# Kernel tuning notes

Hardware: AMD Instinct MI355X
Metric: run time of the kernel (lower is better)

The kernel has to match this reference:

```python
import jax, jax.numpy as jnp
import numpy as np
import math

B, S, D, H = 4, 2048, 512, 8
HD = D // H

def setup_inputs() -> dict:
    key = jax.random.key(0)
    ks = jax.random.split(key, 12)
    s_hd = 1.0 / math.sqrt(HD)
    s_d = 1.0 / math.sqrt(D)
    return {
        "q": jax.random.normal(ks[0], (B, S, D), jnp.float32),
        "k": jax.random.normal(ks[1], (B, S, D), jnp.float32),
        "v": jax.random.normal(ks[2], (B, S, D), jnp.float32),
        # torch nn.Linear(head_dim, head_dim): weight [HD, HD], bias [HD]
        "Wq": jax.random.uniform(ks[3], (HD, HD), jnp.float32, -s_hd, s_hd),
        "bq": jax.random.uniform(ks[4], (HD,), jnp.float32, -s_hd, s_hd),
        "Wk": jax.random.uniform(ks[5], (HD, HD), jnp.float32, -s_hd, s_hd),
        "bk": jax.random.uniform(ks[6], (HD,), jnp.float32, -s_hd, s_hd),
        "Wv": jax.random.uniform(ks[7], (HD, HD), jnp.float32, -s_hd, s_hd),
        "bv": jax.random.uniform(ks[8], (HD,), jnp.float32, -s_hd, s_hd),
        # output projection nn.Linear(d, d)
        "Wo": jax.random.uniform(ks[9], (D, D), jnp.float32, -s_d, s_d),
        "bo": jax.random.uniform(ks[10], (D,), jnp.float32, -s_d, s_d),
        # LayerNorm(d) affine params
        "gamma": jnp.ones((D,), jnp.float32),
        "beta": jnp.zeros((D,), jnp.float32),
    }

def _layernorm(x, gamma, beta, eps=1e-5):
    mu = jnp.mean(x, axis=-1, keepdims=True)
    var = jnp.var(x, axis=-1, keepdims=True)
    return (x - mu) * jax.lax.rsqrt(var + eps) * gamma + beta

def reference(q, k, v, Wq, bq, Wk, bk, Wv, bv, Wo, bo, gamma, beta):
    batch, q_len = q.shape[0], q.shape[1]
    # split heads: [B, L, H, HD]; per-head Linear shares one weight across heads
    Qh = q.reshape(batch, q_len, H, HD) @ Wq.T + bq
    Kh = k.reshape(batch, k.shape[1], H, HD) @ Wk.T + bk
    Vh = v.reshape(batch, v.shape[1], H, HD) @ Wv.T + bv
    # scores scaled by sqrt(d) (faithful to source, NOT sqrt(head_dim))
    scores = jnp.einsum('bqhd,bkhd->bhqk', Qh, Kh) / math.sqrt(D)
    attn = jax.nn.softmax(scores, axis=-1)
    out = jnp.einsum('bhqk,bkhd->bqhd', attn, Vh)
    concat = out.reshape(batch, q_len, D)
    lin = concat @ Wo.T + bo
    # AddNorm quirk: residual added AFTER LayerNorm (dropout = identity in eval)
    return q + _layernorm(lin, gamma, beta)
```

## Files before the change

kernel.cpp:

```cpp
#include <hip/hip_runtime.h>
#include <hip/hip_bf16.h>
#include <math.h>
#include <stdint.h>

#define B 4
#define S 2048
#define D 512
#define H 8
#define HD 64

typedef __attribute__((ext_vector_type(4))) int   int4v;
typedef __attribute__((ext_vector_type(8))) short short8;
typedef __attribute__((ext_vector_type(4))) short short4v;
typedef __attribute__((ext_vector_type(4))) float f32x4;

__device__ __forceinline__ unsigned short bfr(float x) {
    __bf16 h = (__bf16)x;
    union { __bf16 b; unsigned short s; } u; u.b = h; return u.s;
}
__device__ __forceinline__ float b2f(unsigned short s) {
    union { unsigned u; float f; } v; v.u = (unsigned)s << 16; return v.f;
}
__device__ __forceinline__ float ex2(float x) {
#if __has_builtin(__builtin_amdgcn_exp2f)
    return __builtin_amdgcn_exp2f(x);
#else
    return exp2f(x);
#endif
}
__device__ __forceinline__ short8 cvt8(const float* p) {
    float4 f0 = *(const float4*)p;
    float4 f1 = *(const float4*)(p + 4);
    short8 s8;
    s8[0] = (short)bfr(f0.x); s8[1] = (short)bfr(f0.y);
    s8[2] = (short)bfr(f0.z); s8[3] = (short)bfr(f0.w);
    s8[4] = (short)bfr(f1.x); s8[5] = (short)bfr(f1.y);
    s8[6] = (short)bfr(f1.z); s8[7] = (short)bfr(f1.w);
    return s8;
}

#define QSCALE 0.06377229601488305f
#define MFIX 4.0f

typedef const __attribute__((address_space(1))) unsigned char g8_t;
typedef __attribute__((address_space(3))) unsigned char l8_t;
__device__ __forceinline__ void gl_lds16(const unsigned short* g, unsigned short* l) {
#if __has_builtin(__builtin_amdgcn_global_load_lds)
    __builtin_amdgcn_global_load_lds((g8_t*)g, (l8_t*)l, 16, 0, 0);
#else
    int lane = threadIdx.x & 63;
    ((int4v*)l)[lane] = *(const int4v*)g;
#endif
}

__global__ __launch_bounds__(256) void qkv_mfma_kernel(
    const float* __restrict__ q, const float* __restrict__ k,
    const float* __restrict__ v,
    const float* __restrict__ Wq, const float* __restrict__ bq,
    const float* __restrict__ Wk, const float* __restrict__ bk,
    const float* __restrict__ Wv, const float* __restrict__ bv,
    const float* __restrict__ Wo, unsigned short* __restrict__ WoB,
    unsigned short* __restrict__ Qh, unsigned short* __restrict__ Kh,
    unsigned short* __restrict__ VtG)
{
    const int t = threadIdx.x;
    if (blockIdx.x >= 3072) {
        int i = (blockIdx.x - 3072) * 1024 + t * 4;
        float4 f = *(const float4*)(Wo + i);
        short4v s;
        s[0] = (short)bfr(f.x); s[1] = (short)bfr(f.y);
        s[2] = (short)bfr(f.z); s[3] = (short)bfr(f.w);
        *(short4v*)(WoB + i) = s;
        return;
    }

    const int L = t & 63, w = t >> 6;
    const int c = L & 15, qd = L >> 4;
    const int task = blockIdx.x * 4 + w;
    const int st = task & 127;
    const int h  = (task >> 7) & 7;
    const int b  = (task >> 10) & 3;
    const int x  = task >> 12;

    const float* Wf     = (x == 0) ? Wq : (x == 1) ? Wk : Wv;
    const float* bias_p = (x == 0) ? bq : (x == 1) ? bk : bv;
    const float* X      = (x == 0) ? q  : (x == 1) ? k  : v;

    const float* xrow = X + ((size_t)(b * S + st * 16 + c)) * D + h * HD;
    short8 af[2];
    #pragma unroll
    for (int kc = 0; kc < 2; ++kc) af[kc] = cvt8(xrow + kc * 32 + 8 * qd);

    if (x < 2) {
        f32x4 acc[4];
        #pragma unroll
        for (int nt = 0; nt < 4; ++nt) {
            float bv_ = bias_p[16 * nt + c];
            acc[nt] = (f32x4){bv_, bv_, bv_, bv_};
            short8 b0 = cvt8(Wf + (16 * nt + c) * HD + 8 * qd);
            short8 b1 = cvt8(Wf + (16 * nt + c) * HD + 32 + 8 * qd);
            acc[nt] = __builtin_amdgcn_mfma_f32_16x16x32_bf16(af[0], b0, acc[nt], 0, 0, 0);
            acc[nt] = __builtin_amdgcn_mfma_f32_16x16x32_bf16(af[1], b1, acc[nt], 0, 0, 0);
        }
        unsigned short* O = ((x == 0) ? Qh : Kh)
                          + ((size_t)(b * H + h) * S + st * 16) * HD;
        const float sc = (x == 0) ? QSCALE : 1.0f;
        #pragma unroll
        for (int nt = 0; nt < 4; ++nt)
            #pragma unroll
            for (int r = 0; r < 4; ++r)
                O[(4 * qd + r) * HD + 16 * nt + c] = bfr(acc[nt][r] * sc);
    } else {
        f32x4 acc[4];
        #pragma unroll
        for (int nt = 0; nt < 4; ++nt) {
            float4 bb4 = *(const float4*)(bias_p + 16 * nt + 4 * qd);
            acc[nt] = (f32x4){bb4.x, bb4.y, bb4.z, bb4.w};
            short8 a0 = cvt8(Wf + (16 * nt + c) * HD + 8 * qd);
            short8 a1 = cvt8(Wf + (16 * nt + c) * HD + 32 + 8 * qd);
            acc[nt] = __builtin_amdgcn_mfma_f32_16x16x32_bf16(a0, af[0], acc[nt], 0, 0, 0);
            acc[nt] = __builtin_amdgcn_mfma_f32_16x16x32_bf16(a1, af[1], acc[nt], 0, 0, 0);
        }
        unsigned short* O = VtG + (size_t)(b * H + h) * HD * S;
        #pragma unroll
        for (int nt = 0; nt < 4; ++nt)
            #pragma unroll
            for (int r = 0; r < 4; ++r)
                O[(size_t)(16 * nt + 4 * qd + r) * S + st * 16 + c] = bfr(acc[nt][r]);
    }
}

__global__ __launch_bounds__(256, 4) void attn_kernel(
    const unsigned short* __restrict__ Qh, const unsigned short* __restrict__ Kh,
    const unsigned short* __restrict__ VtG, unsigned short* __restrict__ accPb,
    float* __restrict__ lP)
{
    __shared__ __align__(16) unsigned short Ks[2][4096];
    __shared__ __align__(16) unsigned short Vs[2][4096];

    const int idx = blockIdx.x;
    const int bh = idx & 31;
    const int rem = idx >> 5;
    const int qt = rem >> 1;
    const int ks = rem & 1;
    const int b = bh >> 3, h = bh & 7;
    const int t = threadIdx.x;
    const int w = t >> 6, L = t & 63;
    const int c = L & 15, qd = L >> 4;

    const unsigned short* Kb = Kh + ((size_t)bh * S + ks * 1024) * HD;
    const unsigned short* Vb = VtG + (size_t)bh * HD * S + ks * 1024;

    short8 qf[2][2];
    #pragma unroll
    for (int qg = 0; qg < 2; ++qg)
        #pragma unroll
        for (int kc = 0; kc < 2; ++kc)
            qf[qg][kc] = *(const short8*)(Qh
                + ((size_t)bh * S + qt * 128 + w * 32 + qg * 16 + c) * HD
                + kc * 32 + 8 * qd);

    f32x4 acc[2][4];
    float lrun[2] = {0.f, 0.f};
    #pragma unroll
    for (int qg = 0; qg < 2; ++qg)
        #pragma unroll
        for (int dt = 0; dt < 4; ++dt) acc[qg][dt] = (f32x4){0.f, 0.f, 0.f, 0.f};

    const int sd = t >> 3, sj = t & 7;
    const int sp = sj >> 2, smt = (sj >> 1) & 1;
    const int sqa = (2 * sj) & 3, sqb = (2 * sj + 1) & 3;

    int4v vpre[2];
    #pragma unroll
    for (int i = 0; i < 2; ++i) {
        int bi = w + 4 * i;
        gl_lds16(Kb + (size_t)(16 * (bi >> 1) + c) * HD + (bi & 1) * 32 + qd * 8,
                 &Ks[0][bi * 512]);
        vpre[i] = *(const int4v*)(Vb + (size_t)(sd + 32 * i) * S + 8 * sj);
    }

    for (int it = 0; it < 16; ++it) {
        const int cur = it & 1, nxt = cur ^ 1;
        #pragma unroll
        for (int i = 0; i < 2; ++i) {
            int d = sd + 32 * i;
            int dt = d >> 4, cc = d & 15;
            union { int4v v; short4v h[2]; } u; u.v = vpre[i];
            *(short4v*)&Vs[cur][((dt * 2 + sp) * 64 + sqa * 16 + cc) * 8 + smt * 4] = u.h[0];
            *(short4v*)&Vs[cur][((dt * 2 + sp) * 64 + sqb * 16 + cc) * 8 + smt * 4] = u.h[1];
        }
        __syncthreads();
        if (it + 1 < 16) {
            int n1 = (it + 1) * 64;
            #pragma unroll
            for (int i = 0; i < 2; ++i) {
                int bi = w + 4 * i;
                gl_lds16(Kb + (size_t)(n1 + 16 * (bi >> 1) + c) * HD + (bi & 1) * 32 + qd * 8,
                         &Ks[nxt][bi * 512]);
                vpre[i] = *(const int4v*)(Vb + (size_t)(sd + 32 * i) * S + n1 + 8 * sj);
            }
        }

        const unsigned short* KsC = Ks[cur];
        const unsigned short* VsC = Vs[cur];

        short4v pa[2][4];
        #pragma unroll
        for (int mt = 0; mt < 4; ++mt) {
            short8 a0 = *(const short8*)(KsC + (mt * 2 + 0) * 512 + L * 8);
            short8 a1 = *(const short8*)(KsC + (mt * 2 + 1) * 512 + L * 8);
            #pragma unroll
            for (int qg = 0; qg < 2; ++qg) {
                f32x4 stv = (f32x4){-MFIX, -MFIX, -MFIX, -MFIX};
                stv = __builtin_amdgcn_mfma_f32_16x16x32_bf16(a0, qf[qg][0], stv, 0, 0, 0);
                stv = __builtin_amdgcn_mfma_f32_16x16x32_bf16(a1, qf[qg][1], stv, 0, 0, 0);
                float p0 = ex2(stv[0]), p1 = ex2(stv[1]);
                float p2 = ex2(stv[2]), p3 = ex2(stv[3]);
                lrun[qg] += (p0 + p1) + (p2 + p3);
                short4v p_;
                p_[0] = (short)bfr(p0); p_[1] = (short)bfr(p1);
                p_[2] = (short)bfr(p2); p_[3] = (short)bfr(p3);
                pa[qg][mt] = p_;
            }
        }

        #pragma unroll
        for (int dt = 0; dt < 4; ++dt)
            #pragma unroll
            for (int p = 0; p < 2; ++p) {
                union { short8 v8; short4v h[2]; } u;
                u.v8 = *(const short8*)(VsC + (dt * 2 + p) * 512 + L * 8);
#if __has_builtin(__builtin_amdgcn_mfma_f32_16x16x16bf16_1k)
                #pragma unroll
                for (int qg = 0; qg < 2; ++qg) {
                    acc[qg][dt] = __builtin_amdgcn_mfma_f32_16x16x16bf16_1k(
                        pa[qg][2 * p + 0], u.h[0], acc[qg][dt], 0, 0, 0);
                    acc[qg][dt] = __builtin_amdgcn_mfma_f32_16x16x16bf16_1k(
                        pa[qg][2 * p + 1], u.h[1], acc[qg][dt], 0, 0, 0);
                }
#else
                #pragma unroll
                for (int qg = 0; qg < 2; ++qg) {
                    short8 pz0 = {pa[qg][2 * p + 0][0], pa[qg][2 * p + 0][1],
                                  pa[qg][2 * p + 0][2], pa[qg][2 * p + 0][3], 0, 0, 0, 0};
                    short8 pz1 = {pa[qg][2 * p + 1][0], pa[qg][2 * p + 1][1],
                                  pa[qg][2 * p + 1][2], pa[qg][2 * p + 1][3], 0, 0, 0, 0};
                    short8 v0 = {u.h[0][0], u.h[0][1], u.h[0][2], u.h[0][3], 0, 0, 0, 0};
                    short8 v1 = {u.h[1][0], u.h[1][1], u.h[1][2], u.h[1][3], 0, 0, 0, 0};
                    acc[qg][dt] = __builtin_amdgcn_mfma_f32_16x16x32_bf16(pz0, v0, acc[qg][dt], 0, 0, 0);
                    acc[qg][dt] = __builtin_amdgcn_mfma_f32_16x16x32_bf16(pz1, v1, acc[qg][dt], 0, 0, 0);
                }
#endif
            }
    }

    const int q0 = qt * 128 + w * 32;
    unsigned short* accPp = accPb + (size_t)ks * ((size_t)B * S * D)
                          + ((size_t)b * S + q0) * D + h * HD;
    #pragma unroll
    for (int qg = 0; qg < 2; ++qg) {
        float lr = lrun[qg];
        lr += __shfl_xor(lr, 16);
        lr += __shfl_xor(lr, 32);
        if (qd == 0)
            lP[(size_t)ks * ((size_t)B * H * S) + (size_t)bh * S + q0 + qg * 16 + c] = lr;
        #pragma unroll
        for (int dt = 0; dt < 4; ++dt)
            #pragma unroll
            for (int r = 0; r < 4; ++r)
                accPp[(size_t)(qg * 16 + 4 * qd + r) * D + 16 * dt + c]
                    = bfr(acc[qg][dt][r]);
    }
}

__global__ __launch_bounds__(512) void oproj_ln_kernel(
    const unsigned short* __restrict__ accPb, const float* __restrict__ lP,
    const unsigned short* __restrict__ WoB,
    const float* __restrict__ bo, const float* __restrict__ gamma,
    const float* __restrict__ beta, const float* __restrict__ qin,
    float* __restrict__ out)
{
    __shared__ __align__(16) unsigned short As[16 * 520];
    __shared__ float red[2][8][16];
    __shared__ float linv_s[16][8];

    const int t = threadIdx.x;
    const int r0 = blockIdx.x * 16;
    const int w = t >> 6, L = t & 63;
    const int c = L & 15, qd = L >> 4;
    const int n0 = w * 64;
    const size_t NEh = (size_t)B * S * D;
    const size_t BHS = (size_t)B * H * S;

    if (t < 128) {
        int row = t >> 3, hh = t & 7;
        int bb = r0 >> 11;
        int ss = (r0 & (S - 1)) + row;
        float l0 = lP[(size_t)(bb * H + hh) * S + ss];
        float l1 = lP[BHS + (size_t)(bb * H + hh) * S + ss];
        linv_s[row][hh] = 1.f / (l0 + l1);
    }
    __syncthreads();

    #pragma unroll
    for (int i = 0; i < 4; ++i) {
        int flat = t + 512 * i;
        int row = flat >> 7, cg = flat & 127;
        int col = cg * 4;
        size_t gi = (size_t)(r0 + row) * D + col;
        short4v a0 = *(const short4v*)(accPb + gi);
        short4v a1 = *(const short4v*)(accPb + NEh + gi);
        float li = linv_s[row][col >> 6];
        short4v s;
        #pragma unroll
        for (int j = 0; j < 4; ++j)
            s[j] = (short)bfr((b2f((unsigned short)a0[j])
                             + b2f((unsigned short)a1[j])) * li);
        *(short4v*)&As[row * 520 + col] = s;
    }
    __syncthreads();

    f32x4 acc[4];
    #pragma unroll
    for (int nt = 0; nt < 4; ++nt) {
        float bv_ = bo[n0 + 16 * nt + c];
        acc[nt] = (f32x4){bv_, bv_, bv_, bv_};
    }

    for (int kc = 0; kc < 16; ++kc) {
        short8 a0 = *(const short8*)&As[c * 520 + kc * 32 + 8 * qd];
        #pragma unroll
        for (int nt = 0; nt < 4; ++nt) {
            short8 bf = *(const short8*)(WoB + (size_t)(n0 + 16 * nt + c) * D
                                         + kc * 32 + 8 * qd);
            acc[nt] = __builtin_amdgcn_mfma_f32_16x16x32_bf16(a0, bf, acc[nt], 0, 0, 0);
        }
    }

    float sm[4], sq[4];
    #pragma unroll
    for (int r = 0; r < 4; ++r) { sm[r] = 0.f; sq[r] = 0.f; }
    #pragma unroll
    for (int nt = 0; nt < 4; ++nt)
        #pragma unroll
        for (int r = 0; r < 4; ++r) {
            float x_ = acc[nt][r];
            sm[r] += x_; sq[r] += x_ * x_;
        }
    #pragma unroll
    for (int mask = 1; mask <= 8; mask <<= 1)
        #pragma unroll
        for (int r = 0; r < 4; ++r) {
            sm[r] += __shfl_xor(sm[r], mask);
            sq[r] += __shfl_xor(sq[r], mask);
        }
    if (c == 0) {
        #pragma unroll
        for (int r = 0; r < 4; ++r) {
            red[0][w][4 * qd + r] = sm[r];
            red[1][w][4 * qd + r] = sq[r];
        }
    }
    __syncthreads();

    float mu[4], rs[4];
    #pragma unroll
    for (int r = 0; r < 4; ++r) {
        int m_ = 4 * qd + r;
        float s_ = 0.f, q_ = 0.f;
        #pragma unroll
        for (int w_ = 0; w_ < 8; ++w_) { s_ += red[0][w_][m_]; q_ += red[1][w_][m_]; }
        float mu_ = s_ * (1.f / D);
        float var = q_ * (1.f / D) - mu_ * mu_;
        mu[r] = mu_;
        rs[r] = rsqrtf(var + 1e-5f);
    }

    #pragma unroll
    for (int nt = 0; nt < 4; ++nt) {
        int n = n0 + 16 * nt + c;
        float g = gamma[n], be = beta[n];
        #pragma unroll
        for (int r = 0; r < 4; ++r) {
            size_t gi = (size_t)(r0 + 4 * qd + r) * D + n;
            out[gi] = qin[gi] + (acc[nt][r] - mu[r]) * rs[r] * g + be;
        }
    }
}

extern "C" void kernel_launch(void* const* d_in, const int* in_sizes, int n_in,
                              void* d_out, int out_size, void* d_ws, size_t ws_size,
                              hipStream_t stream) {
    const float* q     = (const float*)d_in[0];
    const float* k     = (const float*)d_in[1];
    const float* v     = (const float*)d_in[2];
    const float* Wq    = (const float*)d_in[3];
    const float* bq    = (const float*)d_in[4];
    const float* Wk    = (const float*)d_in[5];
    const float* bk    = (const float*)d_in[6];
    const float* Wv    = (const float*)d_in[7];
    const float* bv    = (const float*)d_in[8];
    const float* Wo    = (const float*)d_in[9];
    const float* bo    = (const float*)d_in[10];
    const float* gamma = (const float*)d_in[11];
    const float* beta  = (const float*)d_in[12];
    float* out = (float*)d_out;

    const size_t NE = (size_t)B * S * D;
    unsigned short* wsu = (unsigned short*)d_ws;
    unsigned short* Qh    = wsu;
    unsigned short* Kh    = wsu + NE;
    unsigned short* VtG   = wsu + 2 * NE;
    unsigned short* WoB   = wsu + 3 * NE;
    unsigned short* accPb = WoB + (size_t)D * D;
    float* lP = (float*)(accPb + 2 * NE);

    hipLaunchKernelGGL(qkv_mfma_kernel, dim3(3072 + 256), dim3(256), 0, stream,
                       q, k, v, Wq, bq, Wk, bk, Wv, bv, Wo, WoB, Qh, Kh, VtG);
    hipLaunchKernelGGL(attn_kernel, dim3(1024), dim3(256), 0, stream,
                       Qh, Kh, VtG, accPb, lP);
    hipLaunchKernelGGL(oproj_ln_kernel, dim3(B * S / 16), dim3(512), 0, stream,
                       accPb, lP, WoB, bo, gamma, beta, q, out);
}
```

Measured before the change: 217.6 us.

## Stage QKV weights in LDS and double row tile in output projection

In the QKV kernel, each block now loads and converts the 64x64 weight into shared memory once and keeps the bf16 fragments in registers. Each wave then processes two 16-row tiles, so the grid halves and the repeated per-wave global weight loads go away. The output-projection/LayerNorm kernel now handles 32 rows per block with 1024 threads, so each Wo fragment feeds two MFMAs, and the row-stat reduction moves to shared memory with an extra barrier. The trade-offs are a larger block size and fewer blocks, which may lower occupancy and load balance.

Result: faster. 192.5 us (-11.6%).

```diff
diff --git a/kernel.cpp b/kernel.cpp
--- a/kernel.cpp
+++ b/kernel.cpp
@@ -64,8 +64,9 @@
     unsigned short* __restrict__ VtG)
 {
     const int t = threadIdx.x;
-    if (blockIdx.x >= 3072) {
-        int i = (blockIdx.x - 3072) * 1024 + t * 4;
+    const int bid = blockIdx.x;
+    if (bid >= 1536) {
+        int i = (bid - 1536) * 1024 + t * 4;
         float4 f = *(const float4*)(Wo + i);
         short4v s;
         s[0] = (short)bfr(f.x); s[1] = (short)bfr(f.y);
@@ -74,59 +75,90 @@
         return;
     }
 
+    __shared__ __align__(16) unsigned short Wl[64 * 72];
+
+    const int x   = bid / 512;
+    const int r_  = bid - x * 512;
+    const int bh  = r_ >> 4;
+    const int stg = r_ & 15;
+    const int b = bh >> 3, h = bh & 7;
     const int L = t & 63, w = t >> 6;
     const int c = L & 15, qd = L >> 4;
-    const int task = blockIdx.x * 4 + w;
-    const int st = task & 127;
-    const int h  = (task >> 7) & 7;
-    const int b  = (task >> 10) & 3;
-    const int x  = task >> 12;
 
     const float* Wf     = (x == 0) ? Wq : (x == 1) ? Wk : Wv;
     const float* bias_p = (x == 0) ? bq : (x == 1) ? bk : bv;
     const float* X      = (x == 0) ? q  : (x == 1) ? k  : v;
 
-    const float* xrow = X + ((size_t)(b * S + st * 16 + c)) * D + h * HD;
-    short8 af[2];
-    #pragma unroll
-    for (int kc = 0; kc < 2; ++kc) af[kc] = cvt8(xrow + kc * 32 + 8 * qd);
+    {
+        int base = t * 16;
+        int row = t >> 2, col = (t & 3) * 16;
+        short8 s0 = cvt8(Wf + base);
+        short8 s1 = cvt8(Wf + base + 8);
+        *(short8*)&Wl[row * 72 + col]     = s0;
+        *(short8*)&Wl[row * 72 + col + 8] = s1;
+    }
+    __syncthreads();
+
+    short8 wf[4][2];
+    #pragma unroll
+    for (int nt = 0; nt < 4; ++nt)
+        #pragma unroll
+        for (int kc = 0; kc < 2; ++kc)
+            wf[nt][kc] = *(const short8*)&Wl[(16 * nt + c) * 72 + kc * 32 + 8 * qd];
 
     if (x < 2) {
-        f32x4 acc[4];
-        #pragma unroll
-        for (int nt = 0; nt < 4; ++nt) {
-            float bv_ = bias_p[16 * nt + c];
-            acc[nt] = (f32x4){bv_, bv_, bv_, bv_};
-            short8 b0 = cvt8(Wf + (16 * nt + c) * HD + 8 * qd);
-            short8 b1 = cvt8(Wf + (16 * nt + c) * HD + 32 + 8 * qd);
-            acc[nt] = __builtin_amdgcn_mfma_f32_16x16x32_bf16(af[0], b0, acc[nt], 0, 0, 0);
-            acc[nt] = __builtin_amdgcn_mfma_f32_16x16x32_bf16(af[1], b1, acc[nt], 0, 0, 0);
-        }
-        unsigned short* O = ((x == 0) ? Qh : Kh)
-                          + ((size_t)(b * H + h) * S + st * 16) * HD;
+        float bias[4];
+        #pragma unroll
+        for (int nt = 0; nt < 4; ++nt) bias[nt] = bias_p[16 * nt + c];
         const float sc = (x == 0) ? QSCALE : 1.0f;
         #pragma unroll
-        for (int nt = 0; nt < 4; ++nt)
-            #pragma unroll
-            for (int r = 0; r < 4; ++r)
-                O[(4 * qd + r) * HD + 16 * nt + c] = bfr(acc[nt][r] * sc);
+        for (int ti = 0; ti < 2; ++ti) {
+            const int st = stg * 8 + w * 2 + ti;
+            const float* xrow = X + ((size_t)(b * S + st * 16 + c)) * D + h * HD;
+            short8 af0 = cvt8(xrow + 8 * qd);
+            short8 af1 = cvt8(xrow + 32 + 8 * qd);
+            f32x4 acc[4];
+            #pragma unroll
+            for (int nt = 0; nt < 4; ++nt) {
+                acc[nt] = (f32x4){bias[nt], bias[nt], bias[nt], bias[nt]};
+                acc[nt] = __builtin_amdgcn_mfma_f32_16x16x32_bf16(af0, wf[nt][0], acc[nt], 0, 0, 0);
+                acc[nt] = __builtin_amdgcn_mfma_f32_16x16x32_bf16(af1, wf[nt][1], acc[nt], 0, 0, 0);
+            }
+            unsigned short* O = ((x == 0) ? Qh : Kh)
+                              + ((size_t)(b * H + h) * S + st * 16) * HD;
+            #pragma unroll
+            for (int nt = 0; nt < 4; ++nt)
+                #pragma unroll
+                for (int r = 0; r < 4; ++r)
+                    O[(4 * qd + r) * HD + 16 * nt + c] = bfr(acc[nt][r] * sc);
+        }
     } else {
-        f32x4 acc[4];
+        f32x4 bias4[4];
         #pragma unroll
         for (int nt = 0; nt < 4; ++nt) {
             float4 bb4 = *(const float4*)(bias_p + 16 * nt + 4 * qd);
-            acc[nt] = (f32x4){bb4.x, bb4.y, bb4.z, bb4.w};
-            short8 a0 = cvt8(Wf + (16 * nt + c) * HD + 8 * qd);
-            short8 a1 = cvt8(Wf + (16 * nt + c) * HD + 32 + 8 * qd);
-            acc[nt] = __builtin_amdgcn_mfma_f32_16x16x32_bf16(a0, af[0], acc[nt], 0, 0, 0);
-            acc[nt] = __builtin_amdgcn_mfma_f32_16x16x32_bf16(a1, af[1], acc[nt], 0, 0, 0);
-        }
-        unsigned short* O = VtG + (size_t)(b * H + h) * HD * S;
-        #pragma unroll
-        for (int nt = 0; nt < 4; ++nt)
-            #pragma unroll
-            for (int r = 0; r < 4; ++r)
-                O[(size_t)(16 * nt + 4 * qd + r) * S + st * 16 + c] = bfr(acc[nt][r]);
+            bias4[nt] = (f32x4){bb4.x, bb4.y, bb4.z, bb4.w};
+        }
+        #pragma unroll
+        for (int ti = 0; ti < 2; ++ti) {
+            const int st = stg * 8 + w * 2 + ti;
+            const float* xrow = X + ((size_t)(b * S + st * 16 + c)) * D + h * HD;
+            short8 af0 = cvt8(xrow + 8 * qd);
+            short8 af1 = cvt8(xrow + 32 + 8 * qd);
+            f32x4 acc[4];
+            #pragma unroll
+            for (int nt = 0; nt < 4; ++nt) {
+                acc[nt] = bias4[nt];
+                acc[nt] = __builtin_amdgcn_mfma_f32_16x16x32_bf16(wf[nt][0], af0, acc[nt], 0, 0, 0);
+                acc[nt] = __builtin_amdgcn_mfma_f32_16x16x32_bf16(wf[nt][1], af1, acc[nt], 0, 0, 0);
+            }
+            unsigned short* O = VtG + (size_t)(b * H + h) * HD * S;
+            #pragma unroll
+            for (int nt = 0; nt < 4; ++nt)
+                #pragma unroll
+                for (int r = 0; r < 4; ++r)
+                    O[(size_t)(16 * nt + 4 * qd + r) * S + st * 16 + c] = bfr(acc[nt][r]);
+        }
     }
 }
 
@@ -274,26 +306,27 @@
     }
 }
 
-__global__ __launch_bounds__(512) void oproj_ln_kernel(
+__global__ __launch_bounds__(1024) void oproj_ln_kernel(
     const unsigned short* __restrict__ accPb, const float* __restrict__ lP,
     const unsigned short* __restrict__ WoB,
     const float* __restrict__ bo, const float* __restrict__ gamma,
     const float* __restrict__ beta, const float* __restrict__ qin,
     float* __restrict__ out)
 {
-    __shared__ __align__(16) unsigned short As[16 * 520];
-    __shared__ float red[2][8][16];
-    __shared__ float linv_s[16][8];
+    __shared__ __align__(16) unsigned short As[32 * 520];
+    __shared__ float red[2][32][17];
+    __shared__ float linv_s[32][8];
+    __shared__ float mu_s2[32], rs_s2[32];
 
     const int t = threadIdx.x;
-    const int r0 = blockIdx.x * 16;
+    const int r0 = blockIdx.x * 32;
     const int w = t >> 6, L = t & 63;
     const int c = L & 15, qd = L >> 4;
-    const int n0 = w * 64;
+    const int n0 = w * 32;
     const size_t NEh = (size_t)B * S * D;
     const size_t BHS = (size_t)B * H * S;
 
-    if (t < 128) {
+    if (t < 256) {
         int row = t >> 3, hh = t & 7;
         int bb = r0 >> 11;
         int ss = (r0 & (S - 1)) + row;
@@ -305,7 +338,7 @@
 
     #pragma unroll
     for (int i = 0; i < 4; ++i) {
-        int flat = t + 512 * i;
+        int flat = t + 1024 * i;
         int row = flat >> 7, cg = flat & 127;
         int col = cg * 4;
         size_t gi = (size_t)(r0 + row) * D + col;
@@ -321,71 +354,83 @@
     }
     __syncthreads();
 
-    f32x4 acc[4];
-    #pragma unroll
-    for (int nt = 0; nt < 4; ++nt) {
+    f32x4 acc[2][2];
+    #pragma unroll
+    for (int nt = 0; nt < 2; ++nt) {
         float bv_ = bo[n0 + 16 * nt + c];
-        acc[nt] = (f32x4){bv_, bv_, bv_, bv_};
+        acc[0][nt] = (f32x4){bv_, bv_, bv_, bv_};
+        acc[1][nt] = (f32x4){bv_, bv_, bv_, bv_};
     }
 
     for (int kc = 0; kc < 16; ++kc) {
         short8 a0 = *(const short8*)&As[c * 520 + kc * 32 + 8 * qd];
-        #pragma unroll
-        for (int nt = 0; nt < 4; ++nt) {
+        short8 a1 = *(const short8*)&As[(16 + c) * 520 + kc * 32 + 8 * qd];
+        #pragma unroll
+        for (int nt = 0; nt < 2; ++nt) {
             short8 bf = *(const short8*)(WoB + (size_t)(n0 + 16 * nt + c) * D
                                          + kc * 32 + 8 * qd);
-            acc[nt] = __builtin_amdgcn_mfma_f32_16x16x32_bf16(a0, bf, acc[nt], 0, 0, 0);
-        }
-    }
-
-    float sm[4], sq[4];
-    #pragma unroll
-    for (int r = 0; r < 4; ++r) { sm[r] = 0.f; sq[r] = 0.f; }
-    #pragma unroll
-    for (int nt = 0; nt < 4; ++nt)
-        #pragma unroll
-        for (int r = 0; r < 4; ++r) {
-            float x_ = acc[nt][r];
-            sm[r] += x_; sq[r] += x_ * x_;
-        }
+            acc[0][nt] = __builtin_amdgcn_mfma_f32_16x16x32_bf16(a0, bf, acc[0][nt], 0, 0, 0);
+            acc[1][nt] = __builtin_amdgcn_mfma_f32_16x16x32_bf16(a1, bf, acc[1][nt], 0, 0, 0);
+        }
+    }
+
+    float sm[2][4], sq[2][4];
+    #pragma unroll
+    for (int mt = 0; mt < 2; ++mt)
+        #pragma unroll
+        for (int r = 0; r < 4; ++r) { sm[mt][r] = 0.f; sq[mt][r] = 0.f; }
+    #pragma unroll
+    for (int mt = 0; mt < 2; ++mt)
+        #pragma unroll
+        for (int nt = 0; nt < 2; ++nt)
+            #pragma unroll
+            for (int r = 0; r < 4; ++r) {
+                float x_ = acc[mt][nt][r];
+                sm[mt][r] += x_; sq[mt][r] += x_ * x_;
+            }
     #pragma unroll
     for (int mask = 1; mask <= 8; mask <<= 1)
         #pragma unroll
-        for (int r = 0; r < 4; ++r) {
-            sm[r] += __shfl_xor(sm[r], mask);
-            sq[r] += __shfl_xor(sq[r], mask);
-        }
+        for (int mt = 0; mt < 2; ++mt)
+            #pragma unroll
+            for (int r = 0; r < 4; ++r) {
+                sm[mt][r] += __shfl_xor(sm[mt][r], mask);
+                sq[mt][r] += __shfl_xor(sq[mt][r], mask);
+            }
     if (c == 0) {
         #pragma unroll
-        for (int r = 0; r < 4; ++r) {
-            red[0][w][4 * qd + r] = sm[r];
-            red[1][w][4 * qd + r] = sq[r];
-        }
+        for (int mt = 0; mt < 2; ++mt)
+            #pragma unroll
+            for (int r = 0; r < 4; ++r) {
+                red[0][mt * 16 + 4 * qd + r][w] = sm[mt][r];
+                red[1][mt * 16 + 4 * qd + r][w] = sq[mt][r];
+            }
     }
     __syncthreads();
 
-    float mu[4], rs[4];
-    #pragma unroll
-    for (int r = 0; r < 4; ++r) {
-        int m_ = 4 * qd + r;
+    if (t < 32) {
         float s_ = 0.f, q_ = 0.f;
         #pragma unroll
-        for (int w_ = 0; w_ < 8; ++w_) { s_ += red[0][w_][m_]; q_ += red[1][w_][m_]; }
+        for (int w_ = 0; w_ < 16; ++w_) { s_ += red[0][t][w_]; q_ += red[1][t][w_]; }
         float mu_ = s_ * (1.f / D);
         float var = q_ * (1.f / D) - mu_ * mu_;
-        mu[r] = mu_;
-        rs[r] = rsqrtf(var + 1e-5f);
-    }
-
-    #pragma unroll
-    for (int nt = 0; nt < 4; ++nt) {
+        mu_s2[t] = mu_;
+        rs_s2[t] = rsqrtf(var + 1e-5f);
+    }
+    __syncthreads();
+
+    #pragma unroll
+    for (int nt = 0; nt < 2; ++nt) {
         int n = n0 + 16 * nt + c;
         float g = gamma[n], be = beta[n];
         #pragma unroll
-        for (int r = 0; r < 4; ++r) {
-            size_t gi = (size_t)(r0 + 4 * qd + r) * D + n;
-            out[gi] = qin[gi] + (acc[nt][r] - mu[r]) * rs[r] * g + be;
-        }
+        for (int mt = 0; mt < 2; ++mt)
+            #pragma unroll
+            for (int r = 0; r < 4; ++r) {
+                int m = mt * 16 + 4 * qd + r;
+                size_t gi = (size_t)(r0 + m) * D + n;
+                out[gi] = qin[gi] + (acc[mt][nt][r] - mu_s2[m]) * rs_s2[m] * g + be;
+            }
     }
 }
 
@@ -416,10 +461,10 @@
     unsigned short* accPb = WoB + (size_t)D * D;
     float* lP = (float*)(accPb + 2 * NE);
 
-    hipLaunchKernelGGL(qkv_mfma_kernel, dim3(3072 + 256), dim3(256), 0, stream,
+    hipLaunchKernelGGL(qkv_mfma_kernel, dim3(1536 + 256), dim3(256), 0, stream,
                        q, k, v, Wq, bq, Wk, bk, Wv, bv, Wo, WoB, Qh, Kh, VtG);
     hipLaunchKernelGGL(attn_kernel, dim3(1024), dim3(256), 0, stream,
                        Qh, Kh, VtG, accPb, lP);
-    hipLaunchKernelGGL(oproj_ln_kernel, dim3(B * S / 16), dim3(512), 0, stream,
+    hipLaunchKernelGGL(oproj_ln_kernel, dim3(B * S / 32), dim3(1024), 0, stream,
                        accPb, lP, WoB, bo, gamma, beta, q, out);
 }
```
